# Optimization experiments

Hardware: AMD Instinct MI355X
Metric: run time of the kernel (lower is better)

Reference implementation:

```python
import jax, jax.numpy as jnp
import numpy as np

B, N, D, M, H = 2, 65536, 512, 128, 32  # batch, points, d_model, modes, temp hidden
LN_EPS = 1e-5
MIN_NORM = 1e-6


def setup_inputs() -> dict:
    key = jax.random.key(0)
    ks = jax.random.split(key, 7)
    x = jax.random.normal(ks[0], (B, N, D), jnp.float32)
    mass = jax.random.uniform(ks[1], (B, N, 1), jnp.float32)
    ln_g = jnp.ones((D,), jnp.float32)
    ln_b = jnp.zeros((D,), jnp.float32)
    # lin: orthogonal-init weight in torch; any full-rank matrix gives same math
    W_lin = jax.random.normal(ks[2], (M, D), jnp.float32) / np.sqrt(D)
    b_lin = jax.random.uniform(ks[3], (M,), jnp.float32, -1.0 / np.sqrt(D), 1.0 / np.sqrt(D))
    # temp_proj: Linear(D,H,bias=False) -> GELU -> Linear(H,1)
    W_t1 = jax.random.normal(ks[4], (H, D), jnp.float32) / np.sqrt(D)
    W_t2 = jax.random.normal(ks[5], (1, H), jnp.float32) * 0.1
    b_t2 = jnp.ones((1,), jnp.float32)
    return {"x": x, "mass": mass, "ln_g": ln_g, "ln_b": ln_b,
            "W_lin": W_lin, "b_lin": b_lin, "W_t1": W_t1, "W_t2": W_t2, "b_t2": b_t2}


def reference(x, mass, ln_g, ln_b, W_lin, b_lin, W_t1, W_t2, b_t2):
    # LayerNorm over d_model
    mu = jnp.mean(x, axis=-1, keepdims=True)
    var = jnp.mean(jnp.square(x - mu), axis=-1, keepdims=True)
    nx = (x - mu) * jax.lax.rsqrt(var + LN_EPS) * ln_g + ln_b  # (B,N,D)
    # d_model -> modes projection
    logits = jnp.einsum('bnd,md->bnm', nx, W_lin) + b_lin       # (B,N,M)
    # per-point temperature: Linear -> GELU(exact) -> Linear -> softplus, clamp [0.01, 3]
    h = jax.nn.gelu(jnp.einsum('bnd,hd->bnh', nx, W_t1), approximate=False)
    tau = jax.nn.softplus(jnp.einsum('bnh,oh->bno', h, W_t2) + b_t2)  # (B,N,1)
    tau = jnp.clip(tau, 0.01, 3.0)
    # eval-mode gumbel_softmax (no noise): softmax(logits / tau)
    trial_func = jax.nn.softmax(logits / tau, axis=-1)          # (B,N,M)
    trial_in_t = jnp.swapaxes(trial_func * mass, -1, -2)        # (B,M,N)
    inv_trial_norm = 1.0 / (jnp.sum(trial_in_t, axis=-1, keepdims=True) + MIN_NORM)  # (B,M,1)
    return trial_func, trial_in_t, inv_trial_norm
```

## Files before the change

kernel.cpp:

```cpp
#include <hip/hip_runtime.h>
#include <hip/hip_bf16.h>

#define D_ 512
#define M_ 128
#define H_ 32
#define NT_ 160
#define P_ 32
#define NPTS_ 65536
#define NPAD_ 520
#define OPAD_ 165
#define BLKS_PER_B 2048

typedef __attribute__((ext_vector_type(8))) short bf16x8;
typedef __attribute__((ext_vector_type(4))) short short4v;
typedef __attribute__((ext_vector_type(4))) float f32x4;

__device__ __forceinline__ short bf16bits(float f) {
    __hip_bfloat16 h = __float2bfloat16(f);
    return *reinterpret_cast<short*>(&h);
}

__global__ __launch_bounds__(256) void prep_kernel(
    const float* __restrict__ W_lin, const float* __restrict__ W_t1,
    __hip_bfloat16* __restrict__ wcat)
{
    int idx = blockIdx.x * 256 + threadIdx.x;
    if (idx < M_ * D_)       wcat[idx] = __float2bfloat16(W_lin[idx]);
    else if (idx < NT_ * D_) wcat[idx] = __float2bfloat16(W_t1[idx - M_ * D_]);
}

__global__ __launch_bounds__(256, 4) void main_kernel(
    const float* __restrict__ x, const float* __restrict__ mass,
    const float* __restrict__ ln_g, const float* __restrict__ ln_b,
    const float* __restrict__ b_lin, const float* __restrict__ W_t2,
    const float* __restrict__ b_t2, const __hip_bfloat16* __restrict__ wcat,
    float* __restrict__ out_tf, float* __restrict__ out_tit,
    float* __restrict__ part)
{
    __shared__ __align__(16) short nx_s[P_ * NPAD_];
    __shared__ float tau_s[P_];
    float* out_l = reinterpret_cast<float*>(nx_s);

    const int tid  = threadIdx.x;
    const int lane = tid & 63;
    const int wave = tid >> 6;
    const int g0   = blockIdx.x * P_;
    const int b_idx = g0 >> 16;
    const int n0    = g0 & (NPTS_ - 1);

    const int k0 = 4 * lane;
    const int k1 = 256 + 4 * lane;

    float4 v0[8], v1[8];
    const float* rowbase = x + (size_t)(g0 + wave) * D_;
    #pragma unroll
    for (int i = 0; i < 8; ++i) {
        const float* row = rowbase + (size_t)(4 * i) * D_;
        v0[i] = *reinterpret_cast<const float4*>(row + k0);
        v1[i] = *reinterpret_cast<const float4*>(row + k1);
    }

    const float4 gv0 = *reinterpret_cast<const float4*>(ln_g + k0);
    const float4 gv1 = *reinterpret_cast<const float4*>(ln_g + k1);
    const float4 bv0 = *reinterpret_cast<const float4*>(ln_b + k0);
    const float4 bv1 = *reinterpret_cast<const float4*>(ln_b + k1);

    #pragma unroll
    for (int i = 0; i < 8; ++i) {
        const int p = wave + 4 * i;
        float s = v0[i].x + v0[i].y + v0[i].z + v0[i].w
                + v1[i].x + v1[i].y + v1[i].z + v1[i].w;
        float q = v0[i].x*v0[i].x + v0[i].y*v0[i].y + v0[i].z*v0[i].z + v0[i].w*v0[i].w
                + v1[i].x*v1[i].x + v1[i].y*v1[i].y + v1[i].z*v1[i].z + v1[i].w*v1[i].w;
        #pragma unroll
        for (int off = 32; off >= 1; off >>= 1) {
            s += __shfl_xor(s, off);
            q += __shfl_xor(q, off);
        }
        const float mean = s * (1.0f / 512.0f);
        const float var  = q * (1.0f / 512.0f) - mean * mean;
        const float rstd = rsqrtf(var + 1e-5f);

        short4v pk0, pk1;
        pk0.x = bf16bits((v0[i].x - mean) * rstd * gv0.x + bv0.x);
        pk0.y = bf16bits((v0[i].y - mean) * rstd * gv0.y + bv0.y);
        pk0.z = bf16bits((v0[i].z - mean) * rstd * gv0.z + bv0.z);
        pk0.w = bf16bits((v0[i].w - mean) * rstd * gv0.w + bv0.w);
        pk1.x = bf16bits((v1[i].x - mean) * rstd * gv1.x + bv1.x);
        pk1.y = bf16bits((v1[i].y - mean) * rstd * gv1.y + bv1.y);
        pk1.z = bf16bits((v1[i].z - mean) * rstd * gv1.z + bv1.z);
        pk1.w = bf16bits((v1[i].w - mean) * rstd * gv1.w + bv1.w);
        *reinterpret_cast<short4v*>(&nx_s[p * NPAD_ + k0]) = pk0;
        *reinterpret_cast<short4v*>(&nx_s[p * NPAD_ + k1]) = pk1;
    }
    __syncthreads();

    const int pt   = wave >> 1;
    const int ncol = (wave & 1) * 80;
    const int rrow = lane & 15;
    const int quad = lane >> 4;

    f32x4 acc[5];
    #pragma unroll
    for (int i = 0; i < 5; ++i) acc[i] = (f32x4){0.f, 0.f, 0.f, 0.f};

    const short* wg = reinterpret_cast<const short*>(wcat) + (ncol + rrow) * D_ + quad * 8;
    const short* ag = &nx_s[(pt * 16 + rrow) * NPAD_ + quad * 8];

#define BLOAD(i, kt) (*reinterpret_cast<const bf16x8*>(wg + (i) * 16 * D_ + (kt) * 32))

    bf16x8 b0[5], b1[5];
    #pragma unroll
    for (int i = 0; i < 5; ++i) b0[i] = BLOAD(i, 0);

    #pragma unroll
    for (int kp = 0; kp < 8; ++kp) {
        #pragma unroll
        for (int i = 0; i < 5; ++i) b1[i] = BLOAD(i, 2 * kp + 1);
        const bf16x8 a0 = *reinterpret_cast<const bf16x8*>(ag + (2 * kp) * 32);
        #pragma unroll
        for (int i = 0; i < 5; ++i)
            acc[i] = __builtin_amdgcn_mfma_f32_16x16x32_bf16(a0, b0[i], acc[i], 0, 0, 0);
        if (kp < 7) {
            #pragma unroll
            for (int i = 0; i < 5; ++i) b0[i] = BLOAD(i, 2 * kp + 2);
        }
        const bf16x8 a1 = *reinterpret_cast<const bf16x8*>(ag + (2 * kp + 1) * 32);
        #pragma unroll
        for (int i = 0; i < 5; ++i)
            acc[i] = __builtin_amdgcn_mfma_f32_16x16x32_bf16(a1, b1[i], acc[i], 0, 0, 0);
    }
#undef BLOAD
    __syncthreads();

    #pragma unroll
    for (int i = 0; i < 5; ++i) {
        #pragma unroll
        for (int r = 0; r < 4; ++r) {
            out_l[(pt * 16 + quad * 4 + r) * OPAD_ + ncol + i * 16 + rrow] = acc[i][r];
        }
    }
    __syncthreads();

    {
        const int p  = tid >> 3;
        const int j4 = (tid & 7) * 4;
        float s = 0.0f;
        #pragma unroll
        for (int jj = 0; jj < 4; ++jj) {
            const float hv = out_l[p * OPAD_ + M_ + j4 + jj];
            const float ge = 0.5f * hv * (1.0f + erff(hv * 0.70710678118f));
            s += ge * W_t2[j4 + jj];
        }
        s += __shfl_xor(s, 1);
        s += __shfl_xor(s, 2);
        s += __shfl_xor(s, 4);
        if ((tid & 7) == 0) {
            const float xx = s + b_t2[0];
            const float sp = fmaxf(xx, 0.0f) + log1pf(expf(-fabsf(xx)));
            tau_s[p] = fminf(fmaxf(sp, 0.01f), 3.0f);
        }
    }

    {
        const int half = lane >> 5;
        const int c    = lane & 31;
        float bl[4];
        #pragma unroll
        for (int j = 0; j < 4; ++j) bl[j] = b_lin[c + 32 * j];

        #pragma unroll
        for (int it = 0; it < 4; ++it) {
            const int p = wave * 8 + it * 2 + half;
            const int g = g0 + p;
            const float itau = 1.0f / tau_s[p];
            const float mv   = mass[g];
            float z[4];
            #pragma unroll
            for (int j = 0; j < 4; ++j)
                z[j] = (out_l[p * OPAD_ + c + 32 * j] + bl[j]) * itau;
            float mx = fmaxf(fmaxf(z[0], z[1]), fmaxf(z[2], z[3]));
            #pragma unroll
            for (int off = 16; off >= 1; off >>= 1) mx = fmaxf(mx, __shfl_xor(mx, off));
            float e[4];
            #pragma unroll
            for (int j = 0; j < 4; ++j) e[j] = __expf(z[j] - mx);
            float ss = (e[0] + e[1]) + (e[2] + e[3]);
            #pragma unroll
            for (int off = 16; off >= 1; off >>= 1) ss += __shfl_xor(ss, off);
            const float inv = 1.0f / ss;
            #pragma unroll
            for (int j = 0; j < 4; ++j) {
                const float t = e[j] * inv;
                out_tf[(size_t)g * M_ + c + 32 * j] = t;
                out_l[p * OPAD_ + c + 32 * j] = t * mv;
            }
        }
    }
    __syncthreads();

    {
        const int mr = tid >> 3;
        const int pg = tid & 7;
        #pragma unroll
        for (int it = 0; it < 4; ++it) {
            const int m = it * 32 + mr;
            float4 v;
            v.x = out_l[(pg * 4 + 0) * OPAD_ + m];
            v.y = out_l[(pg * 4 + 1) * OPAD_ + m];
            v.z = out_l[(pg * 4 + 2) * OPAD_ + m];
            v.w = out_l[(pg * 4 + 3) * OPAD_ + m];
            *reinterpret_cast<float4*>(
                out_tit + (size_t)b_idx * M_ * NPTS_ + (size_t)m * NPTS_ + n0 + pg * 4) = v;
        }
    }

    if (tid < M_) {
        float s = 0.0f;
        #pragma unroll
        for (int p = 0; p < P_; ++p) s += out_l[p * OPAD_ + tid];
        part[((size_t)(b_idx * M_ + tid)) * BLKS_PER_B + (blockIdx.x & (BLKS_PER_B - 1))] = s;
    }
}

__global__ __launch_bounds__(256) void finish_kernel(
    const float* __restrict__ part, float* __restrict__ out_inv)
{
    __shared__ float wsum[4];
    const int j = blockIdx.x;
    const int t = threadIdx.x;
    const float* row = part + (size_t)j * BLKS_PER_B;
    float s = 0.0f;
    #pragma unroll
    for (int i = 0; i < 8; ++i) s += row[i * 256 + t];
    #pragma unroll
    for (int off = 32; off >= 1; off >>= 1) s += __shfl_xor(s, off);
    if ((t & 63) == 0) wsum[t >> 6] = s;
    __syncthreads();
    if (t == 0) out_inv[j] = 1.0f / (wsum[0] + wsum[1] + wsum[2] + wsum[3] + 1e-6f);
}

extern "C" void kernel_launch(void* const* d_in, const int* in_sizes, int n_in,
                              void* d_out, int out_size, void* d_ws, size_t ws_size,
                              hipStream_t stream) {
    const float* x     = (const float*)d_in[0];
    const float* mass  = (const float*)d_in[1];
    const float* ln_g  = (const float*)d_in[2];
    const float* ln_b  = (const float*)d_in[3];
    const float* W_lin = (const float*)d_in[4];
    const float* b_lin = (const float*)d_in[5];
    const float* W_t1  = (const float*)d_in[6];
    const float* W_t2  = (const float*)d_in[7];
    const float* b_t2  = (const float*)d_in[8];

    __hip_bfloat16* wcat = (__hip_bfloat16*)d_ws;
    float* part          = (float*)((char*)d_ws + NT_ * D_ * 2);

    float* out_tf  = (float*)d_out;
    float* out_tit = out_tf + (size_t)2 * NPTS_ * M_;
    float* out_inv = out_tit + (size_t)2 * NPTS_ * M_;

    prep_kernel<<<(NT_ * D_ + 255) / 256, 256, 0, stream>>>(W_lin, W_t1, wcat);

    const int nblocks = (2 * NPTS_) / P_;
    main_kernel<<<nblocks, 256, 0, stream>>>(x, mass, ln_g, ln_b, b_lin, W_t2, b_t2,
                                             wcat, out_tf, out_tit, part);

    finish_kernel<<<2 * M_, 256, 0, stream>>>(part, out_inv);
}
```

Baseline: 518.0 us.

## Make main kernel persistent and prefetch next tile's x rows during compute

The main kernel now runs a fixed grid of 1024 blocks, and each block loops over four 32-point tiles instead of launching one block per tile. The next tile's x rows are loaded into registers right after the LayerNorm results are written to shared memory, so the global load overlaps the MFMA projection, softmax and stores. The aim is to hide x-load latency and reduce block launch overhead. In exchange, register pressure rises (launch bounds lowered from 4 to 3 blocks per CU), and occupancy and grid parallelism drop.

```diff
diff --git a/kernel.cpp b/kernel.cpp
--- a/kernel.cpp
+++ b/kernel.cpp
@@ -10,6 +10,9 @@
 #define NPAD_ 520
 #define OPAD_ 165
 #define BLKS_PER_B 2048
+#define NTILES 4096
+#define GRID_ 1024
+#define ITERS 4
 
 typedef __attribute__((ext_vector_type(8))) short bf16x8;
 typedef __attribute__((ext_vector_type(4))) short short4v;
@@ -29,7 +32,7 @@
     else if (idx < NT_ * D_) wcat[idx] = __float2bfloat16(W_t1[idx - M_ * D_]);
 }
 
-__global__ __launch_bounds__(256, 4) void main_kernel(
+__global__ __launch_bounds__(256, 3) void main_kernel(
     const float* __restrict__ x, const float* __restrict__ mass,
     const float* __restrict__ ln_g, const float* __restrict__ ln_b,
     const float* __restrict__ b_lin, const float* __restrict__ W_t2,
@@ -44,182 +47,199 @@
     const int tid  = threadIdx.x;
     const int lane = tid & 63;
     const int wave = tid >> 6;
-    const int g0   = blockIdx.x * P_;
-    const int b_idx = g0 >> 16;
-    const int n0    = g0 & (NPTS_ - 1);
 
     const int k0 = 4 * lane;
     const int k1 = 256 + 4 * lane;
-
-    float4 v0[8], v1[8];
-    const float* rowbase = x + (size_t)(g0 + wave) * D_;
-    #pragma unroll
-    for (int i = 0; i < 8; ++i) {
-        const float* row = rowbase + (size_t)(4 * i) * D_;
-        v0[i] = *reinterpret_cast<const float4*>(row + k0);
-        v1[i] = *reinterpret_cast<const float4*>(row + k1);
-    }
 
     const float4 gv0 = *reinterpret_cast<const float4*>(ln_g + k0);
     const float4 gv1 = *reinterpret_cast<const float4*>(ln_g + k1);
     const float4 bv0 = *reinterpret_cast<const float4*>(ln_b + k0);
     const float4 bv1 = *reinterpret_cast<const float4*>(ln_b + k1);
 
-    #pragma unroll
-    for (int i = 0; i < 8; ++i) {
-        const int p = wave + 4 * i;
-        float s = v0[i].x + v0[i].y + v0[i].z + v0[i].w
-                + v1[i].x + v1[i].y + v1[i].z + v1[i].w;
-        float q = v0[i].x*v0[i].x + v0[i].y*v0[i].y + v0[i].z*v0[i].z + v0[i].w*v0[i].w
-                + v1[i].x*v1[i].x + v1[i].y*v1[i].y + v1[i].z*v1[i].z + v1[i].w*v1[i].w;
-        #pragma unroll
-        for (int off = 32; off >= 1; off >>= 1) {
-            s += __shfl_xor(s, off);
-            q += __shfl_xor(q, off);
-        }
-        const float mean = s * (1.0f / 512.0f);
-        const float var  = q * (1.0f / 512.0f) - mean * mean;
-        const float rstd = rsqrtf(var + 1e-5f);
-
-        short4v pk0, pk1;
-        pk0.x = bf16bits((v0[i].x - mean) * rstd * gv0.x + bv0.x);
-        pk0.y = bf16bits((v0[i].y - mean) * rstd * gv0.y + bv0.y);
-        pk0.z = bf16bits((v0[i].z - mean) * rstd * gv0.z + bv0.z);
-        pk0.w = bf16bits((v0[i].w - mean) * rstd * gv0.w + bv0.w);
-        pk1.x = bf16bits((v1[i].x - mean) * rstd * gv1.x + bv1.x);
-        pk1.y = bf16bits((v1[i].y - mean) * rstd * gv1.y + bv1.y);
-        pk1.z = bf16bits((v1[i].z - mean) * rstd * gv1.z + bv1.z);
-        pk1.w = bf16bits((v1[i].w - mean) * rstd * gv1.w + bv1.w);
-        *reinterpret_cast<short4v*>(&nx_s[p * NPAD_ + k0]) = pk0;
-        *reinterpret_cast<short4v*>(&nx_s[p * NPAD_ + k1]) = pk1;
-    }
-    __syncthreads();
-
     const int pt   = wave >> 1;
     const int ncol = (wave & 1) * 80;
     const int rrow = lane & 15;
     const int quad = lane >> 4;
-
-    f32x4 acc[5];
-    #pragma unroll
-    for (int i = 0; i < 5; ++i) acc[i] = (f32x4){0.f, 0.f, 0.f, 0.f};
-
     const short* wg = reinterpret_cast<const short*>(wcat) + (ncol + rrow) * D_ + quad * 8;
     const short* ag = &nx_s[(pt * 16 + rrow) * NPAD_ + quad * 8];
 
+    float4 v0[8], v1[8];
+
+    {
+        const float* rowbase = x + (size_t)(blockIdx.x * P_ + wave) * D_;
+        #pragma unroll
+        for (int i = 0; i < 8; ++i) {
+            const float* row = rowbase + (size_t)(4 * i) * D_;
+            v0[i] = *reinterpret_cast<const float4*>(row + k0);
+            v1[i] = *reinterpret_cast<const float4*>(row + k1);
+        }
+    }
+
+    for (int it = 0; it < ITERS; ++it) {
+        const int tile  = blockIdx.x + it * GRID_;
+        const int g0    = tile * P_;
+        const int b_idx = g0 >> 16;
+        const int n0    = g0 & (NPTS_ - 1);
+
+        #pragma unroll
+        for (int i = 0; i < 8; ++i) {
+            const int p = wave + 4 * i;
+            float s = v0[i].x + v0[i].y + v0[i].z + v0[i].w
+                    + v1[i].x + v1[i].y + v1[i].z + v1[i].w;
+            float q = v0[i].x*v0[i].x + v0[i].y*v0[i].y + v0[i].z*v0[i].z + v0[i].w*v0[i].w
+                    + v1[i].x*v1[i].x + v1[i].y*v1[i].y + v1[i].z*v1[i].z + v1[i].w*v1[i].w;
+            #pragma unroll
+            for (int off = 32; off >= 1; off >>= 1) {
+                s += __shfl_xor(s, off);
+                q += __shfl_xor(q, off);
+            }
+            const float mean = s * (1.0f / 512.0f);
+            const float var  = q * (1.0f / 512.0f) - mean * mean;
+            const float rstd = rsqrtf(var + 1e-5f);
+
+            short4v pk0, pk1;
+            pk0.x = bf16bits((v0[i].x - mean) * rstd * gv0.x + bv0.x);
+            pk0.y = bf16bits((v0[i].y - mean) * rstd * gv0.y + bv0.y);
+            pk0.z = bf16bits((v0[i].z - mean) * rstd * gv0.z + bv0.z);
+            pk0.w = bf16bits((v0[i].w - mean) * rstd * gv0.w + bv0.w);
+            pk1.x = bf16bits((v1[i].x - mean) * rstd * gv1.x + bv1.x);
+            pk1.y = bf16bits((v1[i].y - mean) * rstd * gv1.y + bv1.y);
+            pk1.z = bf16bits((v1[i].z - mean) * rstd * gv1.z + bv1.z);
+            pk1.w = bf16bits((v1[i].w - mean) * rstd * gv1.w + bv1.w);
+            *reinterpret_cast<short4v*>(&nx_s[p * NPAD_ + k0]) = pk0;
+            *reinterpret_cast<short4v*>(&nx_s[p * NPAD_ + k1]) = pk1;
+        }
+        __syncthreads();
+
+        if (it + 1 < ITERS) {
+            const float* rowbase = x + (size_t)((tile + GRID_) * P_ + wave) * D_;
+            #pragma unroll
+            for (int i = 0; i < 8; ++i) {
+                const float* row = rowbase + (size_t)(4 * i) * D_;
+                v0[i] = *reinterpret_cast<const float4*>(row + k0);
+                v1[i] = *reinterpret_cast<const float4*>(row + k1);
+            }
+        }
+
+        f32x4 acc[5];
+        #pragma unroll
+        for (int i = 0; i < 5; ++i) acc[i] = (f32x4){0.f, 0.f, 0.f, 0.f};
+
 #define BLOAD(i, kt) (*reinterpret_cast<const bf16x8*>(wg + (i) * 16 * D_ + (kt) * 32))
 
-    bf16x8 b0[5], b1[5];
-    #pragma unroll
-    for (int i = 0; i < 5; ++i) b0[i] = BLOAD(i, 0);
-
-    #pragma unroll
-    for (int kp = 0; kp < 8; ++kp) {
-        #pragma unroll
-        for (int i = 0; i < 5; ++i) b1[i] = BLOAD(i, 2 * kp + 1);
-        const bf16x8 a0 = *reinterpret_cast<const bf16x8*>(ag + (2 * kp) * 32);
-        #pragma unroll
-        for (int i = 0; i < 5; ++i)
-            acc[i] = __builtin_amdgcn_mfma_f32_16x16x32_bf16(a0, b0[i], acc[i], 0, 0, 0);
-        if (kp < 7) {
-            #pragma unroll
-            for (int i = 0; i < 5; ++i) b0[i] = BLOAD(i, 2 * kp + 2);
-        }
-        const bf16x8 a1 = *reinterpret_cast<const bf16x8*>(ag + (2 * kp + 1) * 32);
-        #pragma unroll
-        for (int i = 0; i < 5; ++i)
-            acc[i] = __builtin_amdgcn_mfma_f32_16x16x32_bf16(a1, b1[i], acc[i], 0, 0, 0);
-    }
+        bf16x8 b0[5], b1[5];
+        #pragma unroll
+        for (int i = 0; i < 5; ++i) b0[i] = BLOAD(i, 0);
+
+        #pragma unroll
+        for (int kp = 0; kp < 8; ++kp) {
+            #pragma unroll
+            for (int i = 0; i < 5; ++i) b1[i] = BLOAD(i, 2 * kp + 1);
+            const bf16x8 a0 = *reinterpret_cast<const bf16x8*>(ag + (2 * kp) * 32);
+            #pragma unroll
+            for (int i = 0; i < 5; ++i)
+                acc[i] = __builtin_amdgcn_mfma_f32_16x16x32_bf16(a0, b0[i], acc[i], 0, 0, 0);
+            if (kp < 7) {
+                #pragma unroll
+                for (int i = 0; i < 5; ++i) b0[i] = BLOAD(i, 2 * kp + 2);
+            }
+            const bf16x8 a1 = *reinterpret_cast<const bf16x8*>(ag + (2 * kp + 1) * 32);
+            #pragma unroll
+            for (int i = 0; i < 5; ++i)
+                acc[i] = __builtin_amdgcn_mfma_f32_16x16x32_bf16(a1, b1[i], acc[i], 0, 0, 0);
+        }
 #undef BLOAD
-    __syncthreads();
-
-    #pragma unroll
-    for (int i = 0; i < 5; ++i) {
-        #pragma unroll
-        for (int r = 0; r < 4; ++r) {
-            out_l[(pt * 16 + quad * 4 + r) * OPAD_ + ncol + i * 16 + rrow] = acc[i][r];
-        }
-    }
-    __syncthreads();
-
-    {
-        const int p  = tid >> 3;
-        const int j4 = (tid & 7) * 4;
-        float s = 0.0f;
-        #pragma unroll
-        for (int jj = 0; jj < 4; ++jj) {
-            const float hv = out_l[p * OPAD_ + M_ + j4 + jj];
-            const float ge = 0.5f * hv * (1.0f + erff(hv * 0.70710678118f));
-            s += ge * W_t2[j4 + jj];
-        }
-        s += __shfl_xor(s, 1);
-        s += __shfl_xor(s, 2);
-        s += __shfl_xor(s, 4);
-        if ((tid & 7) == 0) {
-            const float xx = s + b_t2[0];
-            const float sp = fmaxf(xx, 0.0f) + log1pf(expf(-fabsf(xx)));
-            tau_s[p] = fminf(fmaxf(sp, 0.01f), 3.0f);
-        }
-    }
-
-    {
-        const int half = lane >> 5;
-        const int c    = lane & 31;
-        float bl[4];
-        #pragma unroll
-        for (int j = 0; j < 4; ++j) bl[j] = b_lin[c + 32 * j];
-
-        #pragma unroll
-        for (int it = 0; it < 4; ++it) {
-            const int p = wave * 8 + it * 2 + half;
-            const int g = g0 + p;
-            const float itau = 1.0f / tau_s[p];
-            const float mv   = mass[g];
-            float z[4];
-            #pragma unroll
-            for (int j = 0; j < 4; ++j)
-                z[j] = (out_l[p * OPAD_ + c + 32 * j] + bl[j]) * itau;
-            float mx = fmaxf(fmaxf(z[0], z[1]), fmaxf(z[2], z[3]));
-            #pragma unroll
-            for (int off = 16; off >= 1; off >>= 1) mx = fmaxf(mx, __shfl_xor(mx, off));
-            float e[4];
-            #pragma unroll
-            for (int j = 0; j < 4; ++j) e[j] = __expf(z[j] - mx);
-            float ss = (e[0] + e[1]) + (e[2] + e[3]);
-            #pragma unroll
-            for (int off = 16; off >= 1; off >>= 1) ss += __shfl_xor(ss, off);
-            const float inv = 1.0f / ss;
-            #pragma unroll
-            for (int j = 0; j < 4; ++j) {
-                const float t = e[j] * inv;
-                out_tf[(size_t)g * M_ + c + 32 * j] = t;
-                out_l[p * OPAD_ + c + 32 * j] = t * mv;
-            }
-        }
-    }
-    __syncthreads();
-
-    {
-        const int mr = tid >> 3;
-        const int pg = tid & 7;
-        #pragma unroll
-        for (int it = 0; it < 4; ++it) {
-            const int m = it * 32 + mr;
-            float4 v;
-            v.x = out_l[(pg * 4 + 0) * OPAD_ + m];
-            v.y = out_l[(pg * 4 + 1) * OPAD_ + m];
-            v.z = out_l[(pg * 4 + 2) * OPAD_ + m];
-            v.w = out_l[(pg * 4 + 3) * OPAD_ + m];
-            *reinterpret_cast<float4*>(
-                out_tit + (size_t)b_idx * M_ * NPTS_ + (size_t)m * NPTS_ + n0 + pg * 4) = v;
-        }
-    }
-
-    if (tid < M_) {
-        float s = 0.0f;
-        #pragma unroll
-        for (int p = 0; p < P_; ++p) s += out_l[p * OPAD_ + tid];
-        part[((size_t)(b_idx * M_ + tid)) * BLKS_PER_B + (blockIdx.x & (BLKS_PER_B - 1))] = s;
+        __syncthreads();
+
+        #pragma unroll
+        for (int i = 0; i < 5; ++i) {
+            #pragma unroll
+            for (int r = 0; r < 4; ++r) {
+                out_l[(pt * 16 + quad * 4 + r) * OPAD_ + ncol + i * 16 + rrow] = acc[i][r];
+            }
+        }
+        __syncthreads();
+
+        {
+            const int p  = tid >> 3;
+            const int j4 = (tid & 7) * 4;
+            float s = 0.0f;
+            #pragma unroll
+            for (int jj = 0; jj < 4; ++jj) {
+                const float hv = out_l[p * OPAD_ + M_ + j4 + jj];
+                const float ge = 0.5f * hv * (1.0f + erff(hv * 0.70710678118f));
+                s += ge * W_t2[j4 + jj];
+            }
+            s += __shfl_xor(s, 1);
+            s += __shfl_xor(s, 2);
+            s += __shfl_xor(s, 4);
+            if ((tid & 7) == 0) {
+                const float xx = s + b_t2[0];
+                const float sp = fmaxf(xx, 0.0f) + log1pf(expf(-fabsf(xx)));
+                tau_s[p] = fminf(fmaxf(sp, 0.01f), 3.0f);
+            }
+        }
+
+        {
+            const int half = lane >> 5;
+            const int c    = lane & 31;
+            float bl[4];
+            #pragma unroll
+            for (int j = 0; j < 4; ++j) bl[j] = b_lin[c + 32 * j];
+
+            #pragma unroll
+            for (int itp = 0; itp < 4; ++itp) {
+                const int p = wave * 8 + itp * 2 + half;
+                const int g = g0 + p;
+                const float itau = 1.0f / tau_s[p];
+                const float mv   = mass[g];
+                float z[4];
+                #pragma unroll
+                for (int j = 0; j < 4; ++j)
+                    z[j] = (out_l[p * OPAD_ + c + 32 * j] + bl[j]) * itau;
+                float mx = fmaxf(fmaxf(z[0], z[1]), fmaxf(z[2], z[3]));
+                #pragma unroll
+                for (int off = 16; off >= 1; off >>= 1) mx = fmaxf(mx, __shfl_xor(mx, off));
+                float e[4];
+                #pragma unroll
+                for (int j = 0; j < 4; ++j) e[j] = __expf(z[j] - mx);
+                float ss = (e[0] + e[1]) + (e[2] + e[3]);
+                #pragma unroll
+                for (int off = 16; off >= 1; off >>= 1) ss += __shfl_xor(ss, off);
+                const float inv = 1.0f / ss;
+                #pragma unroll
+                for (int j = 0; j < 4; ++j) {
+                    const float t = e[j] * inv;
+                    out_tf[(size_t)g * M_ + c + 32 * j] = t;
+                    out_l[p * OPAD_ + c + 32 * j] = t * mv;
+                }
+            }
+        }
+        __syncthreads();
+
+        {
+            const int mr = tid >> 3;
+            const int pg = tid & 7;
+            #pragma unroll
+            for (int itp = 0; itp < 4; ++itp) {
+                const int m = itp * 32 + mr;
+                float4 v;
+                v.x = out_l[(pg * 4 + 0) * OPAD_ + m];
+                v.y = out_l[(pg * 4 + 1) * OPAD_ + m];
+                v.z = out_l[(pg * 4 + 2) * OPAD_ + m];
+                v.w = out_l[(pg * 4 + 3) * OPAD_ + m];
+                *reinterpret_cast<float4*>(
+                    out_tit + (size_t)b_idx * M_ * NPTS_ + (size_t)m * NPTS_ + n0 + pg * 4) = v;
+            }
+        }
+
+        if (tid < M_) {
+            float s = 0.0f;
+            #pragma unroll
+            for (int p = 0; p < P_; ++p) s += out_l[p * OPAD_ + tid];
+            part[((size_t)(b_idx * M_ + tid)) * BLKS_PER_B + (tile & (BLKS_PER_B - 1))] = s;
+        }
+        __syncthreads();
     }
 }
 
@@ -262,9 +282,8 @@
 
     prep_kernel<<<(NT_ * D_ + 255) / 256, 256, 0, stream>>>(W_lin, W_t1, wcat);
 
-    const int nblocks = (2 * NPTS_) / P_;
-    main_kernel<<<nblocks, 256, 0, stream>>>(x, mass, ln_g, ln_b, b_lin, W_t2, b_t2,
-                                             wcat, out_tf, out_tit, part);
+    main_kernel<<<GRID_, 256, 0, stream>>>(x, mass, ln_g, ln_b, b_lin, W_t2, b_t2,
+                                           wcat, out_tf, out_tit, part);
 
     finish_kernel<<<2 * M_, 256, 0, stream>>>(part, out_inv);
 }
```

Measured after the change: 817.5 us. 1.58x slower.

## Halve points per block, swizzle LDS tile, atomically accumulate mode-sum partials

Applied to the files above, without the earlier changes.

Each block now handles 16 points with 128 threads instead of 32 points with 256 threads. The goal is lower LDS use per block and more resident blocks, so more memory traffic is in flight. The padded nx tile is replaced by an XOR-swizzled layout to avoid LDS bank conflicts without the padding. Tiles are remapped so two neighbouring tiles share one partial-sum slot, filled with atomicAdd into a buffer that the prep kernel zeroes. This keeps the finish kernel's 2048-slot reduction but adds atomics and a larger prep launch.

```diff
diff --git a/kernel.cpp b/kernel.cpp
--- a/kernel.cpp
+++ b/kernel.cpp
@@ -5,11 +5,11 @@
 #define M_ 128
 #define H_ 32
 #define NT_ 160
-#define P_ 32
+#define P_ 16
 #define NPTS_ 65536
-#define NPAD_ 520
 #define OPAD_ 165
-#define BLKS_PER_B 2048
+#define SLOTS_ 2048
+#define NTILES_ 8192
 
 typedef __attribute__((ext_vector_type(8))) short bf16x8;
 typedef __attribute__((ext_vector_type(4))) short short4v;
@@ -22,14 +22,15 @@
 
 __global__ __launch_bounds__(256) void prep_kernel(
     const float* __restrict__ W_lin, const float* __restrict__ W_t1,
-    __hip_bfloat16* __restrict__ wcat)
+    __hip_bfloat16* __restrict__ wcat, float* __restrict__ part)
 {
     int idx = blockIdx.x * 256 + threadIdx.x;
     if (idx < M_ * D_)       wcat[idx] = __float2bfloat16(W_lin[idx]);
     else if (idx < NT_ * D_) wcat[idx] = __float2bfloat16(W_t1[idx - M_ * D_]);
-}
-
-__global__ __launch_bounds__(256, 4) void main_kernel(
+    if (idx < 2 * M_ * SLOTS_) part[idx] = 0.0f;
+}
+
+__global__ __launch_bounds__(128, 5) void main_kernel(
     const float* __restrict__ x, const float* __restrict__ mass,
     const float* __restrict__ ln_g, const float* __restrict__ ln_b,
     const float* __restrict__ b_lin, const float* __restrict__ W_t2,
@@ -37,25 +38,32 @@
     float* __restrict__ out_tf, float* __restrict__ out_tit,
     float* __restrict__ part)
 {
-    __shared__ __align__(16) short nx_s[P_ * NPAD_];
-    __shared__ float tau_s[P_];
+    __shared__ __align__(16) short nx_s[P_ * D_];
     float* out_l = reinterpret_cast<float*>(nx_s);
+    float* tau_l = out_l + P_ * OPAD_;
+    char*  nxb   = reinterpret_cast<char*>(nx_s);
 
     const int tid  = threadIdx.x;
     const int lane = tid & 63;
     const int wave = tid >> 6;
-    const int g0   = blockIdx.x * P_;
-    const int b_idx = g0 >> 16;
-    const int n0    = g0 & (NPTS_ - 1);
+
+    const int blk  = blockIdx.x;
+    const int ln16 = blk & 15;
+    const int tile = (blk >> 4) * 16 + (ln16 & 7) * 2 + (ln16 >> 3);
+    const int g0    = tile * P_;
+    const int b_idx = tile >> 12;
+    const int n0    = (tile & 4095) * P_;
 
     const int k0 = 4 * lane;
     const int k1 = 256 + 4 * lane;
+    const int c0 = 8 * lane;
+    const int c1 = 512 + 8 * lane;
 
     float4 v0[8], v1[8];
     const float* rowbase = x + (size_t)(g0 + wave) * D_;
     #pragma unroll
     for (int i = 0; i < 8; ++i) {
-        const float* row = rowbase + (size_t)(4 * i) * D_;
+        const float* row = rowbase + (size_t)(2 * i) * D_;
         v0[i] = *reinterpret_cast<const float4*>(row + k0);
         v1[i] = *reinterpret_cast<const float4*>(row + k1);
     }
@@ -67,7 +75,7 @@
 
     #pragma unroll
     for (int i = 0; i < 8; ++i) {
-        const int p = wave + 4 * i;
+        const int p = wave + 2 * i;
         float s = v0[i].x + v0[i].y + v0[i].z + v0[i].w
                 + v1[i].x + v1[i].y + v1[i].z + v1[i].w;
         float q = v0[i].x*v0[i].x + v0[i].y*v0[i].y + v0[i].z*v0[i].z + v0[i].w*v0[i].w
@@ -90,24 +98,26 @@
         pk1.y = bf16bits((v1[i].y - mean) * rstd * gv1.y + bv1.y);
         pk1.z = bf16bits((v1[i].z - mean) * rstd * gv1.z + bv1.z);
         pk1.w = bf16bits((v1[i].w - mean) * rstd * gv1.w + bv1.w);
-        *reinterpret_cast<short4v*>(&nx_s[p * NPAD_ + k0]) = pk0;
-        *reinterpret_cast<short4v*>(&nx_s[p * NPAD_ + k1]) = pk1;
-    }
-    __syncthreads();
-
-    const int pt   = wave >> 1;
-    const int ncol = (wave & 1) * 80;
+        const int swp = (p & 7) << 4;
+        *reinterpret_cast<short4v*>(nxb + p * 1024 + (c0 ^ swp)) = pk0;
+        *reinterpret_cast<short4v*>(nxb + p * 1024 + (c1 ^ swp)) = pk1;
+    }
+    __syncthreads();
+
     const int rrow = lane & 15;
     const int quad = lane >> 4;
+    const int ncol = wave * 80;
+    const int sw   = (rrow & 7) << 4;
 
     f32x4 acc[5];
     #pragma unroll
     for (int i = 0; i < 5; ++i) acc[i] = (f32x4){0.f, 0.f, 0.f, 0.f};
 
     const short* wg = reinterpret_cast<const short*>(wcat) + (ncol + rrow) * D_ + quad * 8;
-    const short* ag = &nx_s[(pt * 16 + rrow) * NPAD_ + quad * 8];
+    const char*  rowb = nxb + rrow * 1024;
 
 #define BLOAD(i, kt) (*reinterpret_cast<const bf16x8*>(wg + (i) * 16 * D_ + (kt) * 32))
+#define ALOAD(kt)    (*reinterpret_cast<const bf16x8*>(rowb + ((quad * 16 + (kt) * 64) ^ sw)))
 
     bf16x8 b0[5], b1[5];
     #pragma unroll
@@ -117,7 +127,7 @@
     for (int kp = 0; kp < 8; ++kp) {
         #pragma unroll
         for (int i = 0; i < 5; ++i) b1[i] = BLOAD(i, 2 * kp + 1);
-        const bf16x8 a0 = *reinterpret_cast<const bf16x8*>(ag + (2 * kp) * 32);
+        const bf16x8 a0 = ALOAD(2 * kp);
         #pragma unroll
         for (int i = 0; i < 5; ++i)
             acc[i] = __builtin_amdgcn_mfma_f32_16x16x32_bf16(a0, b0[i], acc[i], 0, 0, 0);
@@ -125,19 +135,20 @@
             #pragma unroll
             for (int i = 0; i < 5; ++i) b0[i] = BLOAD(i, 2 * kp + 2);
         }
-        const bf16x8 a1 = *reinterpret_cast<const bf16x8*>(ag + (2 * kp + 1) * 32);
+        const bf16x8 a1 = ALOAD(2 * kp + 1);
         #pragma unroll
         for (int i = 0; i < 5; ++i)
             acc[i] = __builtin_amdgcn_mfma_f32_16x16x32_bf16(a1, b1[i], acc[i], 0, 0, 0);
     }
 #undef BLOAD
+#undef ALOAD
     __syncthreads();
 
     #pragma unroll
     for (int i = 0; i < 5; ++i) {
         #pragma unroll
         for (int r = 0; r < 4; ++r) {
-            out_l[(pt * 16 + quad * 4 + r) * OPAD_ + ncol + i * 16 + rrow] = acc[i][r];
+            out_l[(quad * 4 + r) * OPAD_ + ncol + i * 16 + rrow] = acc[i][r];
         }
     }
     __syncthreads();
@@ -158,7 +169,7 @@
         if ((tid & 7) == 0) {
             const float xx = s + b_t2[0];
             const float sp = fmaxf(xx, 0.0f) + log1pf(expf(-fabsf(xx)));
-            tau_s[p] = fminf(fmaxf(sp, 0.01f), 3.0f);
+            tau_l[p] = fminf(fmaxf(sp, 0.01f), 3.0f);
         }
     }
 
@@ -170,10 +181,10 @@
         for (int j = 0; j < 4; ++j) bl[j] = b_lin[c + 32 * j];
 
         #pragma unroll
-        for (int it = 0; it < 4; ++it) {
-            const int p = wave * 8 + it * 2 + half;
+        for (int itp = 0; itp < 4; ++itp) {
+            const int p = wave * 8 + itp * 2 + half;
             const int g = g0 + p;
-            const float itau = 1.0f / tau_s[p];
+            const float itau = 1.0f / tau_l[p];
             const float mv   = mass[g];
             float z[4];
             #pragma unroll
@@ -200,11 +211,11 @@
     __syncthreads();
 
     {
-        const int mr = tid >> 3;
-        const int pg = tid & 7;
-        #pragma unroll
-        for (int it = 0; it < 4; ++it) {
-            const int m = it * 32 + mr;
+        const int mr = tid >> 2;
+        const int pg = tid & 3;
+        #pragma unroll
+        for (int itp = 0; itp < 4; ++itp) {
+            const int m = itp * 32 + mr;
             float4 v;
             v.x = out_l[(pg * 4 + 0) * OPAD_ + m];
             v.y = out_l[(pg * 4 + 1) * OPAD_ + m];
@@ -215,11 +226,12 @@
         }
     }
 
-    if (tid < M_) {
+    {
         float s = 0.0f;
         #pragma unroll
         for (int p = 0; p < P_; ++p) s += out_l[p * OPAD_ + tid];
-        part[((size_t)(b_idx * M_ + tid)) * BLKS_PER_B + (blockIdx.x & (BLKS_PER_B - 1))] = s;
+        const int slot = (tile & 4095) >> 1;
+        atomicAdd(&part[(size_t)(b_idx * M_ + tid) * SLOTS_ + slot], s);
     }
 }
 
@@ -229,7 +241,7 @@
     __shared__ float wsum[4];
     const int j = blockIdx.x;
     const int t = threadIdx.x;
-    const float* row = part + (size_t)j * BLKS_PER_B;
+    const float* row = part + (size_t)j * SLOTS_;
     float s = 0.0f;
     #pragma unroll
     for (int i = 0; i < 8; ++i) s += row[i * 256 + t];
@@ -260,10 +272,9 @@
     float* out_tit = out_tf + (size_t)2 * NPTS_ * M_;
     float* out_inv = out_tit + (size_t)2 * NPTS_ * M_;
 
-    prep_kernel<<<(NT_ * D_ + 255) / 256, 256, 0, stream>>>(W_lin, W_t1, wcat);
-
-    const int nblocks = (2 * NPTS_) / P_;
-    main_kernel<<<nblocks, 256, 0, stream>>>(x, mass, ln_g, ln_b, b_lin, W_t2, b_t2,
+    prep_kernel<<<(2 * M_ * SLOTS_ + 255) / 256, 256, 0, stream>>>(W_lin, W_t1, wcat, part);
+
+    main_kernel<<<NTILES_, 128, 0, stream>>>(x, mass, ln_g, ln_b, b_lin, W_t2, b_t2,
                                              wcat, out_tf, out_tit, part);
 
     finish_kernel<<<2 * M_, 256, 0, stream>>>(part, out_inv);
```

New measurement: 557.1 us. +7.6%, slower.

## Stage x rows through LDS with async global_load_lds and swizzle nx layout

Applied to the files above, without the earlier changes.

Instead of loading all 32 rows of x into registers before LayerNorm, each wave streams its rows through a per-wave LDS staging buffer using global_load_lds, double-issuing the next round while normalising the current one. The padded nx layout is replaced by an XOR-swizzled unpadded layout to avoid bank conflicts on MFMA A-operand reads. LDS use grows to about 48KB per block, so occupancy is lowered from 4 to 3 blocks per CU. The intent is to cut register pressure and overlap global loads with compute, at the cost of fewer resident blocks.

```diff
diff --git a/kernel.cpp b/kernel.cpp
--- a/kernel.cpp
+++ b/kernel.cpp
@@ -7,9 +7,13 @@
 #define NT_ 160
 #define P_ 32
 #define NPTS_ 65536
-#define NPAD_ 520
 #define OPAD_ 165
 #define BLKS_PER_B 2048
+
+#define NX_OFF    0
+#define STAGE_OFF 32768
+#define TAU_OFF   49152
+#define LDS_BYTES 49280
 
 typedef __attribute__((ext_vector_type(8))) short bf16x8;
 typedef __attribute__((ext_vector_type(4))) short short4v;
@@ -19,6 +23,11 @@
     __hip_bfloat16 h = __float2bfloat16(f);
     return *reinterpret_cast<short*>(&h);
 }
+
+#define GLOAD_LDS(gsrc, ldst)                                                        \
+    __builtin_amdgcn_global_load_lds(                                                \
+        (const __attribute__((address_space(1))) void*)(gsrc),                       \
+        (__attribute__((address_space(3))) void*)(ldst), 16, 0, 0)
 
 __global__ __launch_bounds__(256) void prep_kernel(
     const float* __restrict__ W_lin, const float* __restrict__ W_t1,
@@ -29,7 +38,7 @@
     else if (idx < NT_ * D_) wcat[idx] = __float2bfloat16(W_t1[idx - M_ * D_]);
 }
 
-__global__ __launch_bounds__(256, 4) void main_kernel(
+__global__ __launch_bounds__(256, 3) void main_kernel(
     const float* __restrict__ x, const float* __restrict__ mass,
     const float* __restrict__ ln_g, const float* __restrict__ ln_b,
     const float* __restrict__ b_lin, const float* __restrict__ W_t2,
@@ -37,9 +46,10 @@
     float* __restrict__ out_tf, float* __restrict__ out_tit,
     float* __restrict__ part)
 {
-    __shared__ __align__(16) short nx_s[P_ * NPAD_];
-    __shared__ float tau_s[P_];
-    float* out_l = reinterpret_cast<float*>(nx_s);
+    __shared__ __align__(16) char lds[LDS_BYTES];
+    char*  nxb   = lds + NX_OFF;
+    float* out_l = reinterpret_cast<float*>(lds + NX_OFF);
+    float* tau_l = reinterpret_cast<float*>(lds + TAU_OFF);
 
     const int tid  = threadIdx.x;
     const int lane = tid & 63;
@@ -51,63 +61,89 @@
     const int k0 = 4 * lane;
     const int k1 = 256 + 4 * lane;
 
-    float4 v0[8], v1[8];
-    const float* rowbase = x + (size_t)(g0 + wave) * D_;
-    #pragma unroll
-    for (int i = 0; i < 8; ++i) {
-        const float* row = rowbase + (size_t)(4 * i) * D_;
-        v0[i] = *reinterpret_cast<const float4*>(row + k0);
-        v1[i] = *reinterpret_cast<const float4*>(row + k1);
-    }
-
     const float4 gv0 = *reinterpret_cast<const float4*>(ln_g + k0);
     const float4 gv1 = *reinterpret_cast<const float4*>(ln_g + k1);
     const float4 bv0 = *reinterpret_cast<const float4*>(ln_b + k0);
     const float4 bv1 = *reinterpret_cast<const float4*>(ln_b + k1);
 
-    #pragma unroll
-    for (int i = 0; i < 8; ++i) {
-        const int p = wave + 4 * i;
-        float s = v0[i].x + v0[i].y + v0[i].z + v0[i].w
-                + v1[i].x + v1[i].y + v1[i].z + v1[i].w;
-        float q = v0[i].x*v0[i].x + v0[i].y*v0[i].y + v0[i].z*v0[i].z + v0[i].w*v0[i].w
-                + v1[i].x*v1[i].x + v1[i].y*v1[i].y + v1[i].z*v1[i].z + v1[i].w*v1[i].w;
-        #pragma unroll
-        for (int off = 32; off >= 1; off >>= 1) {
-            s += __shfl_xor(s, off);
-            q += __shfl_xor(q, off);
-        }
-        const float mean = s * (1.0f / 512.0f);
-        const float var  = q * (1.0f / 512.0f) - mean * mean;
-        const float rstd = rsqrtf(var + 1e-5f);
-
-        short4v pk0, pk1;
-        pk0.x = bf16bits((v0[i].x - mean) * rstd * gv0.x + bv0.x);
-        pk0.y = bf16bits((v0[i].y - mean) * rstd * gv0.y + bv0.y);
-        pk0.z = bf16bits((v0[i].z - mean) * rstd * gv0.z + bv0.z);
-        pk0.w = bf16bits((v0[i].w - mean) * rstd * gv0.w + bv0.w);
-        pk1.x = bf16bits((v1[i].x - mean) * rstd * gv1.x + bv1.x);
-        pk1.y = bf16bits((v1[i].y - mean) * rstd * gv1.y + bv1.y);
-        pk1.z = bf16bits((v1[i].z - mean) * rstd * gv1.z + bv1.z);
-        pk1.w = bf16bits((v1[i].w - mean) * rstd * gv1.w + bv1.w);
-        *reinterpret_cast<short4v*>(&nx_s[p * NPAD_ + k0]) = pk0;
-        *reinterpret_cast<short4v*>(&nx_s[p * NPAD_ + k1]) = pk1;
-    }
+    char* stw = lds + STAGE_OFF + wave * 4096;
+    const float* xg = x + (size_t)g0 * D_;
+
+#define ISSUE_ROUND(t)                                                               \
+    do {                                                                             \
+        _Pragma("unroll")                                                            \
+        for (int j = 0; j < 2; ++j) {                                                \
+            const float* src = xg + (size_t)(wave * 8 + (t) * 2 + j) * D_ + k0;      \
+            GLOAD_LDS(src,       stw + j * 2048);                                    \
+            GLOAD_LDS(src + 256, stw + j * 2048 + 1024);                             \
+        }                                                                            \
+    } while (0)
+
+    ISSUE_ROUND(0);
+
+    #pragma unroll
+    for (int t = 0; t < 4; ++t) {
+        asm volatile("s_waitcnt vmcnt(0)" ::: "memory");
+        float4 v0[2], v1[2];
+        #pragma unroll
+        for (int j = 0; j < 2; ++j) {
+            v0[j] = *reinterpret_cast<const float4*>(stw + j * 2048 + 16 * lane);
+            v1[j] = *reinterpret_cast<const float4*>(stw + j * 2048 + 1024 + 16 * lane);
+        }
+        asm volatile("s_waitcnt lgkmcnt(0)" ::: "memory");
+        if (t < 3) ISSUE_ROUND(t + 1);
+
+        #pragma unroll
+        for (int j = 0; j < 2; ++j) {
+            const int p = wave * 8 + t * 2 + j;
+            float s = v0[j].x + v0[j].y + v0[j].z + v0[j].w
+                    + v1[j].x + v1[j].y + v1[j].z + v1[j].w;
+            float q = v0[j].x*v0[j].x + v0[j].y*v0[j].y + v0[j].z*v0[j].z + v0[j].w*v0[j].w
+                    + v1[j].x*v1[j].x + v1[j].y*v1[j].y + v1[j].z*v1[j].z + v1[j].w*v1[j].w;
+            #pragma unroll
+            for (int off = 32; off >= 1; off >>= 1) {
+                s += __shfl_xor(s, off);
+                q += __shfl_xor(q, off);
+            }
+            const float mean = s * (1.0f / 512.0f);
+            const float var  = q * (1.0f / 512.0f) - mean * mean;
+            const float rstd = rsqrtf(var + 1e-5f);
+
+            short4v pk0, pk1;
+            pk0.x = bf16bits((v0[j].x - mean) * rstd * gv0.x + bv0.x);
+            pk0.y = bf16bits((v0[j].y - mean) * rstd * gv0.y + bv0.y);
+            pk0.z = bf16bits((v0[j].z - mean) * rstd * gv0.z + bv0.z);
+            pk0.w = bf16bits((v0[j].w - mean) * rstd * gv0.w + bv0.w);
+            pk1.x = bf16bits((v1[j].x - mean) * rstd * gv1.x + bv1.x);
+            pk1.y = bf16bits((v1[j].y - mean) * rstd * gv1.y + bv1.y);
+            pk1.z = bf16bits((v1[j].z - mean) * rstd * gv1.z + bv1.z);
+            pk1.w = bf16bits((v1[j].w - mean) * rstd * gv1.w + bv1.w);
+            const int swp = (p & 7) << 4;
+            const int c0  = 8 * lane;
+            const int c1  = 512 + 8 * lane;
+            *reinterpret_cast<short4v*>(nxb + p * 1024 + (c0 ^ swp)) = pk0;
+            *reinterpret_cast<short4v*>(nxb + p * 1024 + (c1 ^ swp)) = pk1;
+        }
+    }
+#undef ISSUE_ROUND
     __syncthreads();
 
     const int pt   = wave >> 1;
     const int ncol = (wave & 1) * 80;
     const int rrow = lane & 15;
     const int quad = lane >> 4;
+    const int arow = pt * 16 + rrow;
+    const int sw   = (arow & 7) << 4;
 
     f32x4 acc[5];
     #pragma unroll
     for (int i = 0; i < 5; ++i) acc[i] = (f32x4){0.f, 0.f, 0.f, 0.f};
 
-    const short* wg = reinterpret_cast<const short*>(wcat) + (ncol + rrow) * D_ + quad * 8;
-    const short* ag = &nx_s[(pt * 16 + rrow) * NPAD_ + quad * 8];
+    const short* wg   = reinterpret_cast<const short*>(wcat) + (ncol + rrow) * D_ + quad * 8;
+    const char*  rowb = nxb + arow * 1024;
 
 #define BLOAD(i, kt) (*reinterpret_cast<const bf16x8*>(wg + (i) * 16 * D_ + (kt) * 32))
+#define ALOAD(kt)    (*reinterpret_cast<const bf16x8*>(rowb + ((quad * 16 + (kt) * 64) ^ sw)))
 
     bf16x8 b0[5], b1[5];
     #pragma unroll
@@ -117,7 +153,7 @@
     for (int kp = 0; kp < 8; ++kp) {
         #pragma unroll
         for (int i = 0; i < 5; ++i) b1[i] = BLOAD(i, 2 * kp + 1);
-        const bf16x8 a0 = *reinterpret_cast<const bf16x8*>(ag + (2 * kp) * 32);
+        const bf16x8 a0 = ALOAD(2 * kp);
         #pragma unroll
         for (int i = 0; i < 5; ++i)
             acc[i] = __builtin_amdgcn_mfma_f32_16x16x32_bf16(a0, b0[i], acc[i], 0, 0, 0);
@@ -125,12 +161,13 @@
             #pragma unroll
             for (int i = 0; i < 5; ++i) b0[i] = BLOAD(i, 2 * kp + 2);
         }
-        const bf16x8 a1 = *reinterpret_cast<const bf16x8*>(ag + (2 * kp + 1) * 32);
+        const bf16x8 a1 = ALOAD(2 * kp + 1);
         #pragma unroll
         for (int i = 0; i < 5; ++i)
             acc[i] = __builtin_amdgcn_mfma_f32_16x16x32_bf16(a1, b1[i], acc[i], 0, 0, 0);
     }
 #undef BLOAD
+#undef ALOAD
     __syncthreads();
 
     #pragma unroll
@@ -158,7 +195,7 @@
         if ((tid & 7) == 0) {
             const float xx = s + b_t2[0];
             const float sp = fmaxf(xx, 0.0f) + log1pf(expf(-fabsf(xx)));
-            tau_s[p] = fminf(fmaxf(sp, 0.01f), 3.0f);
+            tau_l[p] = fminf(fmaxf(sp, 0.01f), 3.0f);
         }
     }
 
@@ -173,7 +210,7 @@
         for (int it = 0; it < 4; ++it) {
             const int p = wave * 8 + it * 2 + half;
             const int g = g0 + p;
-            const float itau = 1.0f / tau_s[p];
+            const float itau = 1.0f / tau_l[p];
             const float mv   = mass[g];
             float z[4];
             #pragma unroll
```

Measured after the change: 555.6 us. 1.07x slower.
